# Kernel optimization log

Measured on AMD Instinct MI355X. Metric: run time of the kernel, lower is better.

The kernel has to match this reference:

```python
import jax, jax.numpy as jnp
import numpy as np

HIDDEN = 2048
P = 4            # patch_size
OUTC = 16        # out_channels
PROJ_IN = min(HIDDEN, 1024)
OUT_DIM = P * P * OUTC


def setup_inputs() -> dict:
    key = jax.random.key(0)
    ks = jax.random.split(key, 7)
    B, H, W = 8, 4096, HIDDEN
    x = jax.random.normal(ks[0], (B, H, W), dtype=jnp.float32)
    c = jax.random.normal(ks[1], (B, PROJ_IN), dtype=jnp.float32)
    # learned params (original zero-inits linear; use small random for non-trivial test)
    W_proj = jax.random.normal(ks[2], (P * P, PROJ_IN), dtype=jnp.float32) * 0.02
    b_proj = jax.random.normal(ks[3], (P * P,), dtype=jnp.float32) * 0.02
    W_lin = jax.random.normal(ks[4], (OUT_DIM, W), dtype=jnp.float32) * 0.02
    b_lin = jax.random.normal(ks[5], (OUT_DIM,), dtype=jnp.float32) * 0.02
    sz = jnp.full((OUT_DIM,), HIDDEN ** -0.5, dtype=jnp.float32)  # sz_init_scaling * ones
    return {"x": x, "c": c, "W_proj": W_proj, "b_proj": b_proj,
            "W_lin": W_lin, "b_lin": b_lin, "sz": sz}


def adafm_modulate(x, ftime, p):
    B, H, W = x.shape
    # (B, H/p, W/p, p*p) patch layout
    xp = x.reshape(B, H // p, p, W // p, p).transpose(0, 1, 3, 2, 4).reshape(B, H // p, W // p, p * p)
    # fft2 over last two axes (W/p, p*p) — matches torch.fft.fft2 default dims
    fspec = jnp.fft.fft2(xp)
    fspec = ftime[:, None, None, :] * fspec  # broadcast (B,1,1,p*p)
    fout = jnp.fft.ifft2(fspec).real
    fout = fout.reshape(B, H // p, W // p, p, p).transpose(0, 1, 3, 2, 4).reshape(B, H, W)
    return fout


def reference(x, c, W_proj, b_proj, W_lin, b_lin, sz):
    ftime = jax.nn.silu(c) @ W_proj.T + b_proj          # (B, p*p)
    xm = adafm_modulate(x, ftime, P)                    # (B, H, W)
    y = xm @ W_lin.T + b_lin                            # (B, H, p*p*C)
    scale = sz * jnp.float32(HIDDEN ** 0.5)             # sz_init_value / sz_init_scaling = sqrt(hidden)
    return scale * y
```

## Files before the change

### kernel.cpp

```cpp
#include <hip/hip_runtime.h>

typedef unsigned int uint;
typedef unsigned short ushort;
typedef __attribute__((ext_vector_type(4))) float f32x4;
typedef __attribute__((ext_vector_type(8))) short short8;

#define BM 64
#define BN 256
#define BK 64
#define KTOT 2048
#define NSTEP (KTOT / BK)

__device__ __forceinline__ ushort f2bf(float f) {
    uint u = __builtin_bit_cast(uint, f);
    u += 0x7FFFu + ((u >> 16) & 1u);
    return (ushort)(u >> 16);
}

__global__ __launch_bounds__(256) void k_ftime(const float* __restrict__ c,
                                               const float* __restrict__ Wp,
                                               const float* __restrict__ bp,
                                               float* __restrict__ ftime) {
    int blk = blockIdx.x;
    int b = blk >> 4, k = blk & 15;
    int tid = threadIdx.x;
    const float* cb = c + b * 1024;
    const float* wk = Wp + k * 1024;
    float v = 0.f;
    for (int t = tid; t < 1024; t += 256) {
        float z = cb[t];
        v += (z / (1.f + expf(-z))) * wk[t];
    }
    for (int off = 32; off; off >>= 1) v += __shfl_down(v, off);
    __shared__ float red[4];
    if ((tid & 63) == 0) red[tid >> 6] = v;
    __syncthreads();
    if (tid == 0) ftime[blk] = red[0] + red[1] + red[2] + red[3] + bp[k];
}

__global__ __launch_bounds__(128) void k_g(const float* __restrict__ ftime,
                                           float* __restrict__ g) {
    int t = threadIdx.x;
    int b = t >> 4, r = t & 15;
    float s = 0.f;
    for (int k = 0; k < 16; ++k)
        s += ftime[b * 16 + k] * cosf((float)((k * r) & 15) * 0.39269908169872414f);
    g[t] = s * 0.0625f;
}

__global__ __launch_bounds__(256) void k_wcvt(const float* __restrict__ W,
                                              ushort* __restrict__ o) {
    int i = (blockIdx.x * 256 + threadIdx.x) * 4;
    float4 v = *(const float4*)(W + i);
    uint lo = (uint)f2bf(v.x) | ((uint)f2bf(v.y) << 16);
    uint hi = (uint)f2bf(v.z) | ((uint)f2bf(v.w) << 16);
    *(uint2*)(o + i) = make_uint2(lo, hi);
}

__global__ __launch_bounds__(512, 4) void k_gemm(
    const float* __restrict__ x,
    const float* __restrict__ Wl,
    const ushort* __restrict__ Wb,
    const float* __restrict__ blin,
    const float* __restrict__ szv,
    const float* __restrict__ g_ws,
    float* __restrict__ out,
    int use_wb) {

    __shared__ __align__(16) ushort As[BM * BK];
    __shared__ __align__(16) ushort Bs[BN * BK];

    const int tid = threadIdx.x;
    const int lane = tid & 63;
    const int wid = tid >> 6;
    const int m0 = blockIdx.x * BM;
    const int b = m0 >> 12;

    float gv[16];
#pragma unroll
    for (int r = 0; r < 16; ++r) gv[r] = g_ws[b * 16 + r];

    const int wr = wid >> 2;
    const int wc = wid & 3;

    f32x4 acc[2][4];
#pragma unroll
    for (int i = 0; i < 2; ++i)
#pragma unroll
        for (int j = 0; j < 4; ++j) acc[i][j] = (f32x4)0.f;

    const int a_hp = (tid & 255) >> 4;
    const int a_wp = tid & 15;

    for (int kt = 0; kt < NSTEP; ++kt) {
        const int k0g = kt * BK;
        if (tid < 256) {
            const float* xr = x + (size_t)(m0 + 4 * a_hp) * 2048 + k0g + 4 * a_wp;
            float4 r0 = *(const float4*)(xr);
            float4 r1 = *(const float4*)(xr + 2048);
            float4 r2 = *(const float4*)(xr + 4096);
            float4 r3 = *(const float4*)(xr + 6144);
            float xin[16] = {r0.x, r0.y, r0.z, r0.w, r1.x, r1.y, r1.z, r1.w,
                             r2.x, r2.y, r2.z, r2.w, r3.x, r3.y, r3.z, r3.w};
            float xo[16];
#pragma unroll
            for (int n = 0; n < 16; ++n) {
                float s = 0.f;
#pragma unroll
                for (int m = 0; m < 16; ++m) s += gv[(n - m) & 15] * xin[m];
                xo[n] = s;
            }
#pragma unroll
            for (int i = 0; i < 4; ++i) {
                int row = 4 * a_hp + i;
                uint lo = (uint)f2bf(xo[i * 4 + 0]) | ((uint)f2bf(xo[i * 4 + 1]) << 16);
                uint hi = (uint)f2bf(xo[i * 4 + 2]) | ((uint)f2bf(xo[i * 4 + 3]) << 16);
                int off = row * (BK * 2) + ((a_wp * 8) ^ ((row & 7) << 4));
                *(uint2*)((char*)As + off) = make_uint2(lo, hi);
            }
        } else {
            const int tt = tid - 256;
            if (use_wb) {
#pragma unroll
                for (int it = 0; it < 8; ++it) {
                    int chunk = it * 256 + tt;
                    int row = chunk >> 3;
                    int c8 = chunk & 7;
                    short8 v = *(const short8*)(Wb + (size_t)row * 2048 + k0g + c8 * 8);
                    int off = row * (BK * 2) + ((c8 * 16) ^ ((row & 7) << 4));
                    *(short8*)((char*)Bs + off) = v;
                }
            } else {
#pragma unroll
                for (int it = 0; it < 16; ++it) {
                    int chunk = it * 256 + tt;
                    int row = chunk >> 4;
                    int c4 = chunk & 15;
                    float4 v = *(const float4*)(Wl + (size_t)row * 2048 + k0g + c4 * 4);
                    uint lo = (uint)f2bf(v.x) | ((uint)f2bf(v.y) << 16);
                    uint hi = (uint)f2bf(v.z) | ((uint)f2bf(v.w) << 16);
                    int off = row * (BK * 2) + ((c4 * 8) ^ ((row & 7) << 4));
                    *(uint2*)((char*)Bs + off) = make_uint2(lo, hi);
                }
            }
        }
        __syncthreads();

#pragma unroll
        for (int kk = 0; kk < 2; ++kk) {
            const int k0 = kk * 32 + ((lane >> 4) << 3);
            short8 a[2], bb[4];
#pragma unroll
            for (int mf = 0; mf < 2; ++mf) {
                int r = wr * 32 + mf * 16 + (lane & 15);
                int off = r * (BK * 2) + (((k0 * 2)) ^ ((r & 7) << 4));
                a[mf] = *(const short8*)((const char*)As + off);
            }
#pragma unroll
            for (int nf = 0; nf < 4; ++nf) {
                int r = wc * 64 + nf * 16 + (lane & 15);
                int off = r * (BK * 2) + (((k0 * 2)) ^ ((r & 7) << 4));
                bb[nf] = *(const short8*)((const char*)Bs + off);
            }
#pragma unroll
            for (int mf = 0; mf < 2; ++mf)
#pragma unroll
                for (int nf = 0; nf < 4; ++nf)
                    acc[mf][nf] = __builtin_amdgcn_mfma_f32_16x16x32_bf16(
                        a[mf], bb[nf], acc[mf][nf], 0, 0, 0);
        }
        __syncthreads();
    }

#pragma unroll
    for (int nf = 0; nf < 4; ++nf) {
        int col = wc * 64 + nf * 16 + (lane & 15);
        float scale = szv[col] * 45.254833995939045f;
        float bl = blin[col];
#pragma unroll
        for (int mf = 0; mf < 2; ++mf) {
            int row = m0 + wr * 32 + mf * 16 + ((lane >> 4) << 2);
#pragma unroll
            for (int j = 0; j < 4; ++j)
                out[(size_t)(row + j) * 256 + col] = scale * (acc[mf][nf][j] + bl);
        }
    }
}

extern "C" void kernel_launch(void* const* d_in, const int* in_sizes, int n_in,
                              void* d_out, int out_size, void* d_ws, size_t ws_size,
                              hipStream_t stream) {
    const float* x  = (const float*)d_in[0];
    const float* c  = (const float*)d_in[1];
    const float* Wp = (const float*)d_in[2];
    const float* bp = (const float*)d_in[3];
    const float* Wl = (const float*)d_in[4];
    const float* bl = (const float*)d_in[5];
    const float* sz = (const float*)d_in[6];
    float* out = (float*)d_out;

    float* wsf = (float*)d_ws;
    float* ftime = wsf;
    float* g = wsf + 128;
    ushort* wbf = (ushort*)(wsf + 256);
    size_t need = 256 * sizeof(float) + (size_t)256 * 2048 * sizeof(ushort);
    int use_wb = (ws_size >= need) ? 1 : 0;

    k_ftime<<<128, 256, 0, stream>>>(c, Wp, bp, ftime);
    k_g<<<1, 128, 0, stream>>>(ftime, g);
    if (use_wb) k_wcvt<<<512, 256, 0, stream>>>(Wl, wbf);
    k_gemm<<<512, 512, 0, stream>>>(x, Wl, use_wb ? wbf : (const ushort*)nullptr,
                                    bl, sz, g, out, use_wb);
}
```

Before: 146.8 us.

## Prefetch operands in registers with double-buffered weight tile and split modulation

Drops the separate bf16 weight-conversion kernel. The GEMM now reads fp32 W_lin directly and converts it to bf16 while staging into shared memory. Global loads for the next K-step of x and W are issued into registers before the current step's MFMA work, and the weight tile is double-buffered in LDS, so load latency overlaps compute. Modulation work is also split across all 512 threads (two threads per patch, each doing half) instead of only 256 threads. The cost is more LDS per block (about 72KB), which may lower occupancy, plus twice the global/L2 traffic for the weight since it is now read as fp32 by every block.

```diff
diff --git a/kernel.cpp b/kernel.cpp
--- a/kernel.cpp
+++ b/kernel.cpp
@@ -5,16 +5,10 @@
 typedef __attribute__((ext_vector_type(4))) float f32x4;
 typedef __attribute__((ext_vector_type(8))) short short8;
 
-#define BM 64
-#define BN 256
-#define BK 64
-#define KTOT 2048
-#define NSTEP (KTOT / BK)
-
-__device__ __forceinline__ ushort f2bf(float f) {
+__device__ __forceinline__ uint f2bf(float f) {
     uint u = __builtin_bit_cast(uint, f);
     u += 0x7FFFu + ((u >> 16) & 1u);
-    return (ushort)(u >> 16);
+    return u >> 16;
 }
 
 __global__ __launch_bounds__(256) void k_ftime(const float* __restrict__ c,
@@ -48,129 +42,151 @@
     g[t] = s * 0.0625f;
 }
 
-__global__ __launch_bounds__(256) void k_wcvt(const float* __restrict__ W,
-                                              ushort* __restrict__ o) {
-    int i = (blockIdx.x * 256 + threadIdx.x) * 4;
-    float4 v = *(const float4*)(W + i);
-    uint lo = (uint)f2bf(v.x) | ((uint)f2bf(v.y) << 16);
-    uint hi = (uint)f2bf(v.z) | ((uint)f2bf(v.w) << 16);
-    *(uint2*)(o + i) = make_uint2(lo, hi);
-}
-
-__global__ __launch_bounds__(512, 4) void k_gemm(
+__device__ __forceinline__ void mod_half(const float (&gv)[16],
+                                         const float4 (&q)[4],
+                                         ushort* Asp, int hp, int wp, int half) {
+    float xin[16] = {q[0].x, q[0].y, q[0].z, q[0].w,
+                     q[1].x, q[1].y, q[1].z, q[1].w,
+                     q[2].x, q[2].y, q[2].z, q[2].w,
+                     q[3].x, q[3].y, q[3].z, q[3].w};
+#pragma unroll
+    for (int i2 = 0; i2 < 2; ++i2) {
+        int i = half * 2 + i2;
+        float xo[4];
+#pragma unroll
+        for (int jj = 0; jj < 4; ++jj) {
+            int n = i * 4 + jj;
+            float s = 0.f;
+#pragma unroll
+            for (int m = 0; m < 16; ++m) s += gv[(n - m) & 15] * xin[m];
+            xo[jj] = s;
+        }
+        int row = 4 * hp + i;
+        uint lo = f2bf(xo[0]) | (f2bf(xo[1]) << 16);
+        uint hi = f2bf(xo[2]) | (f2bf(xo[3]) << 16);
+        int off = row * 128 + ((wp * 8) ^ ((row & 7) << 4));
+        *(uint2*)((char*)Asp + off) = make_uint2(lo, hi);
+    }
+}
+
+__device__ __forceinline__ void mfma_step(const ushort* Ap, const ushort* Bp,
+                                          int lane, int wr, int wc,
+                                          f32x4 (&acc)[2][4]) {
+#pragma unroll
+    for (int kk = 0; kk < 2; ++kk) {
+        const int kb = kk * 64 + ((lane >> 4) << 4);
+        short8 av[2], bv[4];
+#pragma unroll
+        for (int mf = 0; mf < 2; ++mf) {
+            int r = wr * 32 + mf * 16 + (lane & 15);
+            av[mf] = *(const short8*)((const char*)Ap + r * 128 + (kb ^ ((r & 7) << 4)));
+        }
+#pragma unroll
+        for (int nf = 0; nf < 4; ++nf) {
+            int r = wc * 64 + nf * 16 + (lane & 15);
+            bv[nf] = *(const short8*)((const char*)Bp + r * 128 + (kb ^ ((r & 7) << 4)));
+        }
+#pragma unroll
+        for (int mf = 0; mf < 2; ++mf)
+#pragma unroll
+            for (int nf = 0; nf < 4; ++nf)
+                acc[mf][nf] = __builtin_amdgcn_mfma_f32_16x16x32_bf16(
+                    av[mf], bv[nf], acc[mf][nf], 0, 0, 0);
+    }
+}
+
+__global__ __launch_bounds__(512, 4) void k_gemm4(
     const float* __restrict__ x,
     const float* __restrict__ Wl,
-    const ushort* __restrict__ Wb,
     const float* __restrict__ blin,
     const float* __restrict__ szv,
     const float* __restrict__ g_ws,
-    float* __restrict__ out,
-    int use_wb) {
-
-    __shared__ __align__(16) ushort As[BM * BK];
-    __shared__ __align__(16) ushort Bs[BN * BK];
+    float* __restrict__ out) {
+
+    __shared__ __align__(16) ushort As[64 * 64];
+    __shared__ __align__(16) ushort Bs[2][256 * 64];
 
     const int tid = threadIdx.x;
     const int lane = tid & 63;
     const int wid = tid >> 6;
-    const int m0 = blockIdx.x * BM;
+    const int m0 = blockIdx.x * 64;
     const int b = m0 >> 12;
 
     float gv[16];
 #pragma unroll
     for (int r = 0; r < 16; ++r) gv[r] = g_ws[b * 16 + r];
 
-    const int wr = wid >> 2;
-    const int wc = wid & 3;
-
+    const int wr = wid >> 2, wc = wid & 3;
     f32x4 acc[2][4];
 #pragma unroll
     for (int i = 0; i < 2; ++i)
 #pragma unroll
         for (int j = 0; j < 4; ++j) acc[i][j] = (f32x4)0.f;
 
-    const int a_hp = (tid & 255) >> 4;
-    const int a_wp = tid & 15;
-
-    for (int kt = 0; kt < NSTEP; ++kt) {
-        const int k0g = kt * BK;
-        if (tid < 256) {
-            const float* xr = x + (size_t)(m0 + 4 * a_hp) * 2048 + k0g + 4 * a_wp;
-            float4 r0 = *(const float4*)(xr);
-            float4 r1 = *(const float4*)(xr + 2048);
-            float4 r2 = *(const float4*)(xr + 4096);
-            float4 r3 = *(const float4*)(xr + 6144);
-            float xin[16] = {r0.x, r0.y, r0.z, r0.w, r1.x, r1.y, r1.z, r1.w,
-                             r2.x, r2.y, r2.z, r2.w, r3.x, r3.y, r3.z, r3.w};
-            float xo[16];
-#pragma unroll
-            for (int n = 0; n < 16; ++n) {
-                float s = 0.f;
-#pragma unroll
-                for (int m = 0; m < 16; ++m) s += gv[(n - m) & 15] * xin[m];
-                xo[n] = s;
-            }
-#pragma unroll
-            for (int i = 0; i < 4; ++i) {
-                int row = 4 * a_hp + i;
-                uint lo = (uint)f2bf(xo[i * 4 + 0]) | ((uint)f2bf(xo[i * 4 + 1]) << 16);
-                uint hi = (uint)f2bf(xo[i * 4 + 2]) | ((uint)f2bf(xo[i * 4 + 3]) << 16);
-                int off = row * (BK * 2) + ((a_wp * 8) ^ ((row & 7) << 4));
-                *(uint2*)((char*)As + off) = make_uint2(lo, hi);
-            }
-        } else {
-            const int tt = tid - 256;
-            if (use_wb) {
-#pragma unroll
-                for (int it = 0; it < 8; ++it) {
-                    int chunk = it * 256 + tt;
-                    int row = chunk >> 3;
-                    int c8 = chunk & 7;
-                    short8 v = *(const short8*)(Wb + (size_t)row * 2048 + k0g + c8 * 8);
-                    int off = row * (BK * 2) + ((c8 * 16) ^ ((row & 7) << 4));
-                    *(short8*)((char*)Bs + off) = v;
-                }
-            } else {
-#pragma unroll
-                for (int it = 0; it < 16; ++it) {
-                    int chunk = it * 256 + tt;
-                    int row = chunk >> 4;
-                    int c4 = chunk & 15;
-                    float4 v = *(const float4*)(Wl + (size_t)row * 2048 + k0g + c4 * 4);
-                    uint lo = (uint)f2bf(v.x) | ((uint)f2bf(v.y) << 16);
-                    uint hi = (uint)f2bf(v.z) | ((uint)f2bf(v.w) << 16);
-                    int off = row * (BK * 2) + ((c4 * 8) ^ ((row & 7) << 4));
-                    *(uint2*)((char*)Bs + off) = make_uint2(lo, hi);
-                }
-            }
-        }
+    const int p = tid >> 1;
+    const int hp = p >> 4;
+    const int wp = p & 15;
+    const int half = tid & 1;
+    const float* xbase = x + (size_t)(m0 + 4 * hp) * 2048 + 4 * wp;
+
+    float4 q[4];
+    float4 blo[4], bhi[4];
+
+#define STAGE_LOAD(kt) do { \
+        const float* wb_ = Wl + (size_t)(kt) * 64; \
+        _Pragma("unroll") \
+        for (int it = 0; it < 4; ++it) { \
+            int chunk = it * 512 + tid; \
+            int row_ = chunk >> 3, slot_ = chunk & 7; \
+            const float* src_ = wb_ + (size_t)row_ * 2048 + slot_ * 8; \
+            blo[it] = *(const float4*)(src_); \
+            bhi[it] = *(const float4*)(src_ + 4); \
+        } \
+    } while (0)
+
+#define STAGE_WRITE(pp) do { \
+        _Pragma("unroll") \
+        for (int it = 0; it < 4; ++it) { \
+            int chunk = it * 512 + tid; \
+            int row_ = chunk >> 3, slot_ = chunk & 7; \
+            uint4 pk_; \
+            pk_.x = f2bf(blo[it].x) | (f2bf(blo[it].y) << 16); \
+            pk_.y = f2bf(blo[it].z) | (f2bf(blo[it].w) << 16); \
+            pk_.z = f2bf(bhi[it].x) | (f2bf(bhi[it].y) << 16); \
+            pk_.w = f2bf(bhi[it].z) | (f2bf(bhi[it].w) << 16); \
+            int off_ = row_ * 128 + ((slot_ * 16) ^ ((row_ & 7) << 4)); \
+            *(uint4*)((char*)&Bs[pp][0] + off_) = pk_; \
+        } \
+    } while (0)
+
+#define LOADX(kt) do { \
+        const float* xr_ = xbase + (kt) * 64; \
+        q[0] = *(const float4*)(xr_); \
+        q[1] = *(const float4*)(xr_ + 2048); \
+        q[2] = *(const float4*)(xr_ + 4096); \
+        q[3] = *(const float4*)(xr_ + 6144); \
+    } while (0)
+
+    STAGE_LOAD(0);
+    LOADX(0);
+    STAGE_WRITE(0);
+    mod_half(gv, q, As, hp, wp, half);
+    __syncthreads();
+
+    for (int t = 0; t < 31; ++t) {
+        STAGE_LOAD(t + 1);
+        LOADX(t + 1);
+        mfma_step(As, &Bs[t & 1][0], lane, wr, wc, acc);
         __syncthreads();
-
-#pragma unroll
-        for (int kk = 0; kk < 2; ++kk) {
-            const int k0 = kk * 32 + ((lane >> 4) << 3);
-            short8 a[2], bb[4];
-#pragma unroll
-            for (int mf = 0; mf < 2; ++mf) {
-                int r = wr * 32 + mf * 16 + (lane & 15);
-                int off = r * (BK * 2) + (((k0 * 2)) ^ ((r & 7) << 4));
-                a[mf] = *(const short8*)((const char*)As + off);
-            }
-#pragma unroll
-            for (int nf = 0; nf < 4; ++nf) {
-                int r = wc * 64 + nf * 16 + (lane & 15);
-                int off = r * (BK * 2) + (((k0 * 2)) ^ ((r & 7) << 4));
-                bb[nf] = *(const short8*)((const char*)Bs + off);
-            }
-#pragma unroll
-            for (int mf = 0; mf < 2; ++mf)
-#pragma unroll
-                for (int nf = 0; nf < 4; ++nf)
-                    acc[mf][nf] = __builtin_amdgcn_mfma_f32_16x16x32_bf16(
-                        a[mf], bb[nf], acc[mf][nf], 0, 0, 0);
-        }
+        STAGE_WRITE((t + 1) & 1);
+        mod_half(gv, q, As, hp, wp, half);
         __syncthreads();
     }
+    mfma_step(As, &Bs[1][0], lane, wr, wc, acc);
+
+#undef STAGE_LOAD
+#undef STAGE_WRITE
+#undef LOADX
 
 #pragma unroll
     for (int nf = 0; nf < 4; ++nf) {
@@ -202,13 +218,8 @@
     float* wsf = (float*)d_ws;
     float* ftime = wsf;
     float* g = wsf + 128;
-    ushort* wbf = (ushort*)(wsf + 256);
-    size_t need = 256 * sizeof(float) + (size_t)256 * 2048 * sizeof(ushort);
-    int use_wb = (ws_size >= need) ? 1 : 0;
 
     k_ftime<<<128, 256, 0, stream>>>(c, Wp, bp, ftime);
     k_g<<<1, 128, 0, stream>>>(ftime, g);
-    if (use_wb) k_wcvt<<<512, 256, 0, stream>>>(Wl, wbf);
-    k_gemm<<<512, 512, 0, stream>>>(x, Wl, use_wb ? wbf : (const ushort*)nullptr,
-                                    bl, sz, g, out, use_wb);
-}
+    k_gemm4<<<512, 512, 0, stream>>>(x, Wl, bl, sz, g, out);
+}
```

Result: slower. 314.1 us (+114.0%).
